# Performance work log

Hardware: AMD Instinct MI355X
Metric: run time of the kernel (lower is better)

## Reference

```python
import jax, jax.numpy as jnp
import numpy as np

N_NODES = 100000
N_EDGES = 1600000
IN_F = 256
H1, H2 = 128, 64


def gcn_conv(x, W, b, src, dst, n_nodes):
    """PyG-style GCNConv: add self-loops, symmetric deg normalization,
    transform then scatter-add aggregate, bias after aggregation."""
    loop = jnp.arange(n_nodes)
    s = jnp.concatenate([src, loop])
    d = jnp.concatenate([dst, loop])
    deg = jax.ops.segment_sum(jnp.ones_like(d, x.dtype), d, num_segments=n_nodes)
    dinv = jnp.where(deg > 0, deg ** -0.5, 0.0)
    norm = dinv[s] * dinv[d]                     # [E+N]
    h = x @ W                                    # [N, out]
    msg = h[s] * norm[:, None]                   # [E+N, out]
    out = jax.ops.segment_sum(msg, d, num_segments=n_nodes)
    return out + b


def setup_inputs() -> dict:
    key = jax.random.key(0)
    k = jax.random.split(key, 7)
    x = jax.random.normal(k[0], (N_NODES, IN_F), dtype=jnp.float32)
    edge_index = jax.random.randint(k[1], (2, N_EDGES), 0, N_NODES, dtype=jnp.int64)
    # Glorot-ish init for linear weights (PyG lin has no bias; conv bias separate)
    W1 = jax.random.normal(k[2], (IN_F, H1), dtype=jnp.float32) / np.sqrt(IN_F)
    b1 = jnp.zeros((H1,), dtype=jnp.float32)
    W2 = jax.random.normal(k[3], (H1, H2), dtype=jnp.float32) / np.sqrt(H1)
    b2 = jnp.zeros((H2,), dtype=jnp.float32)
    return {"x": x, "edge_index": edge_index, "W1": W1, "b1": b1, "W2": W2, "b2": b2}


def reference(x, edge_index, W1, b1, W2, b2):
    n = x.shape[0]
    src, dst = edge_index[0], edge_index[1]
    h = gcn_conv(x, W1, b1, src, dst, n)
    h = jax.nn.relu(h)
    # F.dropout(p=0.2, training=self.training): identity in eval mode
    out = gcn_conv(h, W2, b2, src, dst, n)
    return out
```

## Files before the change

### kernel.cpp

```cpp
#include <hip/hip_runtime.h>

#define IN_F 256
#define HID1 128
#define HID2 64
#define NBLK 256
#define RB_LOG 9
#define RB 512

typedef __bf16 bf16x8 __attribute__((ext_vector_type(8)));
typedef float f32x4 __attribute__((ext_vector_type(4)));
typedef unsigned short ushort8 __attribute__((ext_vector_type(8)));
typedef unsigned long long u64;

__device__ inline unsigned short f2bf(float f) {
    unsigned int u = __float_as_uint(f);
    u += 0x7fffu + ((u >> 16) & 1u);
    return (unsigned short)(u >> 16);
}
__device__ inline float bf2f(unsigned short u) {
    return __uint_as_float(((unsigned int)u) << 16);
}

__global__ void detect_kernel(const int* __restrict__ e, long long nOdd, int* flag) {
    long long stride = (long long)gridDim.x * blockDim.x;
    for (long long i = (long long)blockIdx.x * blockDim.x + threadIdx.x; i < nOdd; i += stride) {
        if (e[2 * i + 1] != 0) { *flag = 1; return; }
    }
}

__device__ inline int edge_src(const void* e, const int is32, long long i, int E) {
    return is32 ? ((const int*)e)[i] : (int)((const long long*)e)[i];
}
__device__ inline int edge_dst(const void* e, const int is32, long long i, int E) {
    return is32 ? ((const int*)e)[E + i] : (int)((const long long*)e)[E + i];
}

__global__ __launch_bounds__(256) void p1_count_kernel(const void* __restrict__ e,
                                                       const int* __restrict__ flag,
                                                       int* __restrict__ bhist,
                                                       int N, int E, int nbk, int chunk) {
    __shared__ int hist[256];
    const int is32 = *flag;
    const int blk = blockIdx.x;
    const int t = threadIdx.x;
    for (int j = t; j < nbk; j += 256) hist[j] = 0;
    __syncthreads();
    long long lo = (long long)blk * chunk;
    long long hi = lo + chunk; if (hi > E) hi = E;
    for (long long i = lo + t; i < hi; i += 256) {
        int s = edge_src(e, is32, i, E);
        int d = edge_dst(e, is32, i, E);
        if ((unsigned)s < (unsigned)N && (unsigned)d < (unsigned)N)
            atomicAdd(&hist[d >> RB_LOG], 1);
    }
    __syncthreads();
    for (int j = t; j < nbk; j += 256) bhist[j * NBLK + blk] = hist[j];
}

__global__ __launch_bounds__(256) void p2a_kernel(int* __restrict__ bhist, int* __restrict__ tot) {
    __shared__ int wsums[4], wpre[4];
    const int b = blockIdx.x;
    const int t = threadIdx.x;
    int v = bhist[b * NBLK + t];
    const int lane = t & 63;
    int x = v;
#pragma unroll
    for (int off = 1; off < 64; off <<= 1) {
        int y = __shfl_up(x, off, 64);
        if (lane >= off) x += y;
    }
    if (lane == 63) wsums[t >> 6] = x;
    __syncthreads();
    if (t == 0) { int r = 0; for (int w = 0; w < 4; w++) { wpre[w] = r; r += wsums[w]; } }
    __syncthreads();
    int excl = wpre[t >> 6] + x - v;
    bhist[b * NBLK + t] = excl;
    if (t == 255) tot[b] = excl + v;
}

__global__ void p2b_kernel(const int* __restrict__ tot, int* __restrict__ bstart,
                           int* __restrict__ rowptr, int nbk, int N) {
    if (threadIdx.x == 0 && blockIdx.x == 0) {
        int r = 0;
        for (int i = 0; i < nbk; i++) { bstart[i] = r; r += tot[i]; }
        bstart[nbk] = r;
        rowptr[N] = r;
    }
}

__global__ __launch_bounds__(256) void p3_scatter_kernel(const void* __restrict__ e,
                                                         const int* __restrict__ flag,
                                                         const int* __restrict__ bhist,
                                                         const int* __restrict__ bstart,
                                                         u64* __restrict__ ebuf,
                                                         int N, int E, int nbk, int chunk) {
    __shared__ int cur[256];
    const int is32 = *flag;
    const int blk = blockIdx.x;
    const int t = threadIdx.x;
    for (int j = t; j < nbk; j += 256) cur[j] = bhist[j * NBLK + blk] + bstart[j];
    __syncthreads();
    long long lo = (long long)blk * chunk;
    long long hi = lo + chunk; if (hi > E) hi = E;
    for (long long i = lo + t; i < hi; i += 256) {
        int s = edge_src(e, is32, i, E);
        int d = edge_dst(e, is32, i, E);
        if ((unsigned)s < (unsigned)N && (unsigned)d < (unsigned)N) {
            int p = atomicAdd(&cur[d >> RB_LOG], 1);
            ebuf[p] = ((u64)(unsigned)d << 32) | (unsigned)s;
        }
    }
}

__global__ __launch_bounds__(256) void p4_finalize_kernel(const u64* __restrict__ ebuf,
                                                          const int* __restrict__ bstart,
                                                          int* __restrict__ rowptr,
                                                          float* __restrict__ dinv,
                                                          int* __restrict__ col, int N) {
    __shared__ int cnt[RB];
    __shared__ int lrp[RB];
    __shared__ int wsums[4], wpre[4];
    const int b = blockIdx.x;
    const int t = threadIdx.x;
    const int e0 = bstart[b], e1 = bstart[b + 1];
    const int node0 = b << RB_LOG;
    int nn = N - node0; if (nn > RB) nn = RB;
    for (int j = t; j < RB; j += 256) cnt[j] = 0;
    __syncthreads();
    for (int i = e0 + t; i < e1; i += 256) {
        int d = (int)(ebuf[i] >> 32);
        atomicAdd(&cnt[d - node0], 1);
    }
    __syncthreads();
    int c0 = cnt[2 * t], c1 = cnt[2 * t + 1];
    int s = c0 + c1;
    const int lane = t & 63;
    int x = s;
#pragma unroll
    for (int off = 1; off < 64; off <<= 1) {
        int y = __shfl_up(x, off, 64);
        if (lane >= off) x += y;
    }
    if (lane == 63) wsums[t >> 6] = x;
    __syncthreads();
    if (t == 0) { int r = 0; for (int w = 0; w < 4; w++) { wpre[w] = r; r += wsums[w]; } }
    __syncthreads();
    int excl = wpre[t >> 6] + x - s;
    lrp[2 * t] = excl;
    lrp[2 * t + 1] = excl + c0;
    __syncthreads();
    for (int j = t; j < nn; j += 256) {
        rowptr[node0 + j] = e0 + lrp[j];
        dinv[node0 + j] = rsqrtf((float)(cnt[j] + 1));
    }
    __syncthreads();
    for (int i = e0 + t; i < e1; i += 256) {
        u64 rec = ebuf[i];
        int d = (int)(rec >> 32);
        int p = atomicAdd(&lrp[d - node0], 1);
        col[e0 + p] = (int)(unsigned)rec;
    }
}

__global__ void wbt_kernel(const float* __restrict__ W, unsigned short* __restrict__ Wbt,
                           int K, int C) {
    int t = blockIdx.x * 256 + threadIdx.x;
    if (t >= K * C) return;
    int c = t / K;
    int k = t - c * K;
    Wbt[t] = f2bf(W[k * C + c]);
}

__global__ __launch_bounds__(256) void gemm1_mfma_kernel(const float* __restrict__ x,
                                                         const unsigned short* __restrict__ Wbt,
                                                         unsigned short* __restrict__ hb, int N) {
    __shared__ unsigned short As[64 * 64];
    __shared__ unsigned short Bs[128 * 64];
    const int t = threadIdx.x;
    const int w = t >> 6;
    const int l = t & 63;
    const int lrow = l & 15;
    const int g = l >> 4;
    const int row0 = blockIdx.x * 64;

    f32x4 acc[4][2];
#pragma unroll
    for (int m = 0; m < 4; m++)
#pragma unroll
        for (int n = 0; n < 2; n++) acc[m][n] = (f32x4){0.f, 0.f, 0.f, 0.f};

    for (int kc = 0; kc < 4; kc++) {
        __syncthreads();
#pragma unroll
        for (int it = 0; it < 2; it++) {
            int slot = it * 256 + t;
            int r = slot >> 3;
            int k0 = (slot & 7) * 8;
            int grow = row0 + r;
            float4 v0 = make_float4(0.f, 0.f, 0.f, 0.f), v1 = v0;
            if (grow < N) {
                const float* p = &x[(long long)grow * IN_F + kc * 64 + k0];
                v0 = *(const float4*)p;
                v1 = *(const float4*)(p + 4);
            }
            ushort8 u;
            u[0] = f2bf(v0.x); u[1] = f2bf(v0.y); u[2] = f2bf(v0.z); u[3] = f2bf(v0.w);
            u[4] = f2bf(v1.x); u[5] = f2bf(v1.y); u[6] = f2bf(v1.z); u[7] = f2bf(v1.w);
            *(ushort8*)&As[r * 64 + (k0 ^ ((r & 7) << 3))] = u;
        }
#pragma unroll
        for (int it = 0; it < 4; it++) {
            int slot = it * 256 + t;
            int c = slot >> 3;
            int k0 = (slot & 7) * 8;
            ushort8 u = *(const ushort8*)&Wbt[c * IN_F + kc * 64 + k0];
            *(ushort8*)&Bs[c * 64 + (k0 ^ ((c & 7) << 3))] = u;
        }
        __syncthreads();
#pragma unroll
        for (int ks = 0; ks < 2; ks++) {
            int kk = ks * 32 + g * 8;
            bf16x8 af[4], bfr[2];
#pragma unroll
            for (int m = 0; m < 4; m++) {
                int r = m * 16 + lrow;
                af[m] = *(bf16x8*)&As[r * 64 + (kk ^ ((r & 7) << 3))];
            }
#pragma unroll
            for (int n = 0; n < 2; n++) {
                int c = w * 32 + n * 16 + lrow;
                bfr[n] = *(bf16x8*)&Bs[c * 64 + (kk ^ ((c & 7) << 3))];
            }
#pragma unroll
            for (int m = 0; m < 4; m++)
#pragma unroll
                for (int n = 0; n < 2; n++)
                    acc[m][n] = __builtin_amdgcn_mfma_f32_16x16x32_bf16(af[m], bfr[n], acc[m][n], 0, 0, 0);
        }
    }
#pragma unroll
    for (int m = 0; m < 4; m++) {
        int rbase = row0 + m * 16 + g * 4;
#pragma unroll
        for (int j = 0; j < 4; j++) {
            int grow = rbase + j;
            if (grow < N) {
#pragma unroll
                for (int n = 0; n < 2; n++)
                    hb[(long long)grow * HID1 + w * 32 + n * 16 + lrow] = f2bf(acc[m][n][j]);
            }
        }
    }
}

__global__ __launch_bounds__(256) void gemm2_mfma_kernel(const unsigned short* __restrict__ ab,
                                                         const unsigned short* __restrict__ Wbt,
                                                         unsigned short* __restrict__ hb, int N) {
    __shared__ unsigned short As[64 * 64];
    __shared__ unsigned short Bs[64 * 64];
    const int t = threadIdx.x;
    const int w = t >> 6;
    const int l = t & 63;
    const int lrow = l & 15;
    const int g = l >> 4;
    const int row0 = blockIdx.x * 64;

    f32x4 acc[4];
#pragma unroll
    for (int m = 0; m < 4; m++) acc[m] = (f32x4){0.f, 0.f, 0.f, 0.f};

    for (int kc = 0; kc < 2; kc++) {
        __syncthreads();
#pragma unroll
        for (int it = 0; it < 2; it++) {
            int slot = it * 256 + t;
            int r = slot >> 3;
            int k0 = (slot & 7) * 8;
            int grow = row0 + r;
            ushort8 u = (ushort8){0, 0, 0, 0, 0, 0, 0, 0};
            if (grow < N)
                u = *(const ushort8*)&ab[(long long)grow * HID1 + kc * 64 + k0];
            *(ushort8*)&As[r * 64 + (k0 ^ ((r & 7) << 3))] = u;
        }
#pragma unroll
        for (int it = 0; it < 2; it++) {
            int slot = it * 256 + t;
            int c = slot >> 3;
            int k0 = (slot & 7) * 8;
            ushort8 u = *(const ushort8*)&Wbt[c * HID1 + kc * 64 + k0];
            *(ushort8*)&Bs[c * 64 + (k0 ^ ((c & 7) << 3))] = u;
        }
        __syncthreads();
#pragma unroll
        for (int ks = 0; ks < 2; ks++) {
            int kk = ks * 32 + g * 8;
            bf16x8 af[4], bfr;
#pragma unroll
            for (int m = 0; m < 4; m++) {
                int r = m * 16 + lrow;
                af[m] = *(bf16x8*)&As[r * 64 + (kk ^ ((r & 7) << 3))];
            }
            {
                int c = w * 16 + lrow;
                bfr = *(bf16x8*)&Bs[c * 64 + (kk ^ ((c & 7) << 3))];
            }
#pragma unroll
            for (int m = 0; m < 4; m++)
                acc[m] = __builtin_amdgcn_mfma_f32_16x16x32_bf16(af[m], bfr, acc[m], 0, 0, 0);
        }
    }
#pragma unroll
    for (int m = 0; m < 4; m++) {
        int rbase = row0 + m * 16 + g * 4;
#pragma unroll
        for (int j = 0; j < 4; j++) {
            int grow = rbase + j;
            if (grow < N)
                hb[(long long)grow * HID2 + w * 16 + lrow] = f2bf(acc[m][j]);
        }
    }
}

template <int G, bool RELUBF>
__global__ __launch_bounds__(256) void gather_bf16_kernel(const unsigned short* __restrict__ hb,
                                                          const float* __restrict__ bias,
                                                          const float* __restrict__ dinv,
                                                          const int* __restrict__ rowptr,
                                                          const int* __restrict__ col,
                                                          void* __restrict__ out, int N) {
    long long tid = (long long)blockIdx.x * 256 + threadIdx.x;
    int node = (int)(tid / G);
    int g = (int)(tid % G);
    if (node >= N) return;
    const ushort8* h8 = (const ushort8*)hb;
    float di = dinv[node];
    ushort8 hv = h8[(long long)node * G + g];
    float sum[8];
#pragma unroll
    for (int j = 0; j < 8; j++) sum[j] = di * bf2f(hv[j]);
    int p0 = rowptr[node], p1 = rowptr[node + 1];
    int p = p0;
    for (; p + 3 < p1; p += 4) {
        int s0 = col[p], s1 = col[p + 1], s2 = col[p + 2], s3 = col[p + 3];
        float w0 = dinv[s0], w1 = dinv[s1], w2 = dinv[s2], w3 = dinv[s3];
        ushort8 v0 = h8[(long long)s0 * G + g];
        ushort8 v1 = h8[(long long)s1 * G + g];
        ushort8 v2 = h8[(long long)s2 * G + g];
        ushort8 v3 = h8[(long long)s3 * G + g];
#pragma unroll
        for (int j = 0; j < 8; j++)
            sum[j] += (w0 * bf2f(v0[j]) + w1 * bf2f(v1[j])) +
                      (w2 * bf2f(v2[j]) + w3 * bf2f(v3[j]));
    }
    for (; p < p1; p++) {
        int s0 = col[p];
        float w0 = dinv[s0];
        ushort8 v0 = h8[(long long)s0 * G + g];
#pragma unroll
        for (int j = 0; j < 8; j++) sum[j] += w0 * bf2f(v0[j]);
    }
    float4 b0 = ((const float4*)bias)[g * 2];
    float4 b1 = ((const float4*)bias)[g * 2 + 1];
    float r[8];
    r[0] = b0.x + di * sum[0]; r[1] = b0.y + di * sum[1];
    r[2] = b0.z + di * sum[2]; r[3] = b0.w + di * sum[3];
    r[4] = b1.x + di * sum[4]; r[5] = b1.y + di * sum[5];
    r[6] = b1.z + di * sum[6]; r[7] = b1.w + di * sum[7];
    if (RELUBF) {
        ushort8 u;
#pragma unroll
        for (int j = 0; j < 8; j++) u[j] = f2bf(fmaxf(r[j], 0.f));
        ((ushort8*)out)[(long long)node * G + g] = u;
    } else {
        float4 o0 = make_float4(r[0], r[1], r[2], r[3]);
        float4 o1 = make_float4(r[4], r[5], r[6], r[7]);
        float4* op = (float4*)((float*)out + ((long long)node * G + g) * 8);
        op[0] = o0;
        op[1] = o1;
    }
}

extern "C" void kernel_launch(void* const* d_in, const int* in_sizes, int n_in,
                              void* d_out, int out_size, void* d_ws, size_t ws_size,
                              hipStream_t stream) {
    const float* x  = (const float*)d_in[0];
    const void*  ei = d_in[1];
    const float* W1 = (const float*)d_in[2];
    const float* b1 = (const float*)d_in[3];
    const float* W2 = (const float*)d_in[4];
    const float* b2 = (const float*)d_in[5];
    float* out = (float*)d_out;

    const int N = in_sizes[0] / IN_F;
    const int E = in_sizes[1] / 2;
    const int nbk = (N + RB - 1) >> RB_LOG;
    const int chunk = (E + NBLK - 1) / NBLK;

    char* ws = (char*)d_ws;
    size_t off = 0;
    auto alloc = [&](size_t bytes) -> char* {
        char* p = ws + off;
        off = (off + bytes + 255) & ~(size_t)255;
        return p;
    };
    int*   flag   = (int*)alloc(4);
    int*   bhist  = (int*)alloc((size_t)256 * NBLK * 4);
    int*   tot    = (int*)alloc(256 * 4);
    int*   bstart = (int*)alloc(257 * 4);
    float* dinv   = (float*)alloc((size_t)N * 4);
    int*   rowptr = (int*)alloc((size_t)(N + 1) * 4);
    u64*   ebuf   = (u64*)alloc((size_t)E * 8);
    int*   col    = (int*)alloc((size_t)E * 4);
    unsigned short* w1bt  = (unsigned short*)alloc((size_t)HID1 * IN_F * 2);
    unsigned short* w2bt  = (unsigned short*)alloc((size_t)HID2 * HID1 * 2);
    unsigned short* h1b   = (unsigned short*)alloc((size_t)N * HID1 * 2);
    unsigned short* agg1b = (unsigned short*)alloc((size_t)N * HID1 * 2);
    unsigned short* h2b   = (unsigned short*)alloc((size_t)N * HID2 * 2);

    hipMemsetAsync(flag, 0, sizeof(int), stream);

    detect_kernel<<<1024, 256, 0, stream>>>((const int*)ei, (long long)E, flag);

    p1_count_kernel<<<NBLK, 256, 0, stream>>>(ei, flag, bhist, N, E, nbk, chunk);
    p2a_kernel<<<nbk, 256, 0, stream>>>(bhist, tot);
    p2b_kernel<<<1, 64, 0, stream>>>(tot, bstart, rowptr, nbk, N);
    p3_scatter_kernel<<<NBLK, 256, 0, stream>>>(ei, flag, bhist, bstart, ebuf, N, E, nbk, chunk);
    p4_finalize_kernel<<<nbk, 256, 0, stream>>>(ebuf, bstart, rowptr, dinv, col, N);

    wbt_kernel<<<(HID1 * IN_F + 255) / 256, 256, 0, stream>>>(W1, w1bt, IN_F, HID1);
    wbt_kernel<<<(HID2 * HID1 + 255) / 256, 256, 0, stream>>>(W2, w2bt, HID1, HID2);

    gemm1_mfma_kernel<<<(N + 63) / 64, 256, 0, stream>>>(x, w1bt, h1b, N);
    gather_bf16_kernel<16, true><<<(int)(((long long)N * 16 + 255) / 256), 256, 0, stream>>>(
        h1b, b1, dinv, rowptr, col, agg1b, N);

    gemm2_mfma_kernel<<<(N + 63) / 64, 256, 0, stream>>>(agg1b, w2bt, h2b, N);
    gather_bf16_kernel<8, false><<<(int)(((long long)N * 8 + 255) / 256), 256, 0, stream>>>(
        h2b, b2, dinv, rowptr, col, out, N);
}
```

Measured before the change: 203.7 us.

## Shrink CSR buckets, parallelize bucket scan, merge weight casts, deepen gather unroll

Halves the destination bucket size to 256 nodes, giving more finalize blocks, and rewrites the single-thread bucket prefix scan as a 512-thread wave scan. The two weight transpose launches are merged into one kernel. The dtype detection now samples only the first 4096 edges in a single block. The gather kernel gains an 8-wide unrolled loop with occupancy launch bounds so more neighbor loads are in flight. Risks: the detection shortcut assumes the first edges are representative of the index dtype, and nbk must stay at or below 512.

```diff
diff --git a/kernel.cpp b/kernel.cpp
--- a/kernel.cpp
+++ b/kernel.cpp
@@ -4,8 +4,8 @@
 #define HID1 128
 #define HID2 64
 #define NBLK 256
-#define RB_LOG 9
-#define RB 512
+#define RB_LOG 8
+#define RB 256
 
 typedef __bf16 bf16x8 __attribute__((ext_vector_type(8)));
 typedef float f32x4 __attribute__((ext_vector_type(4)));
@@ -39,7 +39,7 @@
                                                        const int* __restrict__ flag,
                                                        int* __restrict__ bhist,
                                                        int N, int E, int nbk, int chunk) {
-    __shared__ int hist[256];
+    __shared__ int hist[512];
     const int is32 = *flag;
     const int blk = blockIdx.x;
     const int t = threadIdx.x;
@@ -78,13 +78,29 @@
     if (t == 255) tot[b] = excl + v;
 }
 
-__global__ void p2b_kernel(const int* __restrict__ tot, int* __restrict__ bstart,
-                           int* __restrict__ rowptr, int nbk, int N) {
-    if (threadIdx.x == 0 && blockIdx.x == 0) {
-        int r = 0;
-        for (int i = 0; i < nbk; i++) { bstart[i] = r; r += tot[i]; }
-        bstart[nbk] = r;
-        rowptr[N] = r;
+__global__ __launch_bounds__(512) void p2b_kernel(const int* __restrict__ tot,
+                                                  int* __restrict__ bstart,
+                                                  int* __restrict__ rowptr, int nbk, int N) {
+    __shared__ int wsums[8], wpre[8];
+    const int t = threadIdx.x;
+    int v = (t < nbk) ? tot[t] : 0;
+    const int lane = t & 63;
+    int x = v;
+#pragma unroll
+    for (int off = 1; off < 64; off <<= 1) {
+        int y = __shfl_up(x, off, 64);
+        if (lane >= off) x += y;
+    }
+    if (lane == 63) wsums[t >> 6] = x;
+    __syncthreads();
+    if (t == 0) { int r = 0; for (int w = 0; w < 8; w++) { wpre[w] = r; r += wsums[w]; } }
+    __syncthreads();
+    int excl = wpre[t >> 6] + x - v;
+    if (t < nbk) bstart[t] = excl;
+    if (t == 511) {
+        int total = wpre[7] + wsums[7];
+        bstart[nbk] = total;
+        rowptr[N] = total;
     }
 }
 
@@ -94,7 +110,7 @@
                                                          const int* __restrict__ bstart,
                                                          u64* __restrict__ ebuf,
                                                          int N, int E, int nbk, int chunk) {
-    __shared__ int cur[256];
+    __shared__ int cur[512];
     const int is32 = *flag;
     const int blk = blockIdx.x;
     const int t = threadIdx.x;
@@ -125,17 +141,16 @@
     const int e0 = bstart[b], e1 = bstart[b + 1];
     const int node0 = b << RB_LOG;
     int nn = N - node0; if (nn > RB) nn = RB;
-    for (int j = t; j < RB; j += 256) cnt[j] = 0;
+    cnt[t] = 0;
     __syncthreads();
     for (int i = e0 + t; i < e1; i += 256) {
         int d = (int)(ebuf[i] >> 32);
         atomicAdd(&cnt[d - node0], 1);
     }
     __syncthreads();
-    int c0 = cnt[2 * t], c1 = cnt[2 * t + 1];
-    int s = c0 + c1;
+    int v = cnt[t];
     const int lane = t & 63;
-    int x = s;
+    int x = v;
 #pragma unroll
     for (int off = 1; off < 64; off <<= 1) {
         int y = __shfl_up(x, off, 64);
@@ -145,13 +160,11 @@
     __syncthreads();
     if (t == 0) { int r = 0; for (int w = 0; w < 4; w++) { wpre[w] = r; r += wsums[w]; } }
     __syncthreads();
-    int excl = wpre[t >> 6] + x - s;
-    lrp[2 * t] = excl;
-    lrp[2 * t + 1] = excl + c0;
-    __syncthreads();
-    for (int j = t; j < nn; j += 256) {
-        rowptr[node0 + j] = e0 + lrp[j];
-        dinv[node0 + j] = rsqrtf((float)(cnt[j] + 1));
+    int excl = wpre[t >> 6] + x - v;
+    lrp[t] = excl;
+    if (t < nn) {
+        rowptr[node0 + t] = e0 + excl;
+        dinv[node0 + t] = rsqrtf((float)(v + 1));
     }
     __syncthreads();
     for (int i = e0 + t; i < e1; i += 256) {
@@ -162,13 +175,19 @@
     }
 }
 
-__global__ void wbt_kernel(const float* __restrict__ W, unsigned short* __restrict__ Wbt,
-                           int K, int C) {
+__global__ void wbt2_kernel(const float* __restrict__ W1, unsigned short* __restrict__ w1bt,
+                            const float* __restrict__ W2, unsigned short* __restrict__ w2bt) {
     int t = blockIdx.x * 256 + threadIdx.x;
-    if (t >= K * C) return;
-    int c = t / K;
-    int k = t - c * K;
-    Wbt[t] = f2bf(W[k * C + c]);
+    if (t < IN_F * HID1) {
+        int c = t >> 8, k = t & 255;
+        w1bt[t] = f2bf(W1[k * HID1 + c]);
+    } else {
+        int u = t - IN_F * HID1;
+        if (u < HID1 * HID2) {
+            int c = u >> 7, k = u & 127;
+            w2bt[u] = f2bf(W2[k * HID2 + c]);
+        }
+    }
 }
 
 __global__ __launch_bounds__(256) void gemm1_mfma_kernel(const float* __restrict__ x,
@@ -322,12 +341,12 @@
 }
 
 template <int G, bool RELUBF>
-__global__ __launch_bounds__(256) void gather_bf16_kernel(const unsigned short* __restrict__ hb,
-                                                          const float* __restrict__ bias,
-                                                          const float* __restrict__ dinv,
-                                                          const int* __restrict__ rowptr,
-                                                          const int* __restrict__ col,
-                                                          void* __restrict__ out, int N) {
+__global__ __launch_bounds__(256, 8) void gather_bf16_kernel(const unsigned short* __restrict__ hb,
+                                                             const float* __restrict__ bias,
+                                                             const float* __restrict__ dinv,
+                                                             const int* __restrict__ rowptr,
+                                                             const int* __restrict__ col,
+                                                             void* __restrict__ out, int N) {
     long long tid = (long long)blockIdx.x * 256 + threadIdx.x;
     int node = (int)(tid / G);
     int g = (int)(tid % G);
@@ -340,6 +359,21 @@
     for (int j = 0; j < 8; j++) sum[j] = di * bf2f(hv[j]);
     int p0 = rowptr[node], p1 = rowptr[node + 1];
     int p = p0;
+    for (; p + 7 < p1; p += 8) {
+        int sN[8];
+        float wN[8];
+        ushort8 vN[8];
+#pragma unroll
+        for (int q = 0; q < 8; q++) sN[q] = col[p + q];
+#pragma unroll
+        for (int q = 0; q < 8; q++) vN[q] = h8[(long long)sN[q] * G + g];
+#pragma unroll
+        for (int q = 0; q < 8; q++) wN[q] = dinv[sN[q]];
+#pragma unroll
+        for (int q = 0; q < 8; q++)
+#pragma unroll
+            for (int j = 0; j < 8; j++) sum[j] += wN[q] * bf2f(vN[q][j]);
+    }
     for (; p + 3 < p1; p += 4) {
         int s0 = col[p], s1 = col[p + 1], s2 = col[p + 2], s3 = col[p + 3];
         float w0 = dinv[s0], w1 = dinv[s1], w2 = dinv[s2], w3 = dinv[s3];
@@ -404,9 +438,9 @@
         return p;
     };
     int*   flag   = (int*)alloc(4);
-    int*   bhist  = (int*)alloc((size_t)256 * NBLK * 4);
-    int*   tot    = (int*)alloc(256 * 4);
-    int*   bstart = (int*)alloc(257 * 4);
+    int*   bhist  = (int*)alloc((size_t)512 * NBLK * 4);
+    int*   tot    = (int*)alloc(512 * 4);
+    int*   bstart = (int*)alloc(520 * 4);
     float* dinv   = (float*)alloc((size_t)N * 4);
     int*   rowptr = (int*)alloc((size_t)(N + 1) * 4);
     u64*   ebuf   = (u64*)alloc((size_t)E * 8);
@@ -419,16 +453,16 @@
 
     hipMemsetAsync(flag, 0, sizeof(int), stream);
 
-    detect_kernel<<<1024, 256, 0, stream>>>((const int*)ei, (long long)E, flag);
+    long long nOdd = E < 4096 ? (long long)E : 4096;
+    detect_kernel<<<1, 256, 0, stream>>>((const int*)ei, nOdd, flag);
 
     p1_count_kernel<<<NBLK, 256, 0, stream>>>(ei, flag, bhist, N, E, nbk, chunk);
     p2a_kernel<<<nbk, 256, 0, stream>>>(bhist, tot);
-    p2b_kernel<<<1, 64, 0, stream>>>(tot, bstart, rowptr, nbk, N);
+    p2b_kernel<<<1, 512, 0, stream>>>(tot, bstart, rowptr, nbk, N);
     p3_scatter_kernel<<<NBLK, 256, 0, stream>>>(ei, flag, bhist, bstart, ebuf, N, E, nbk, chunk);
     p4_finalize_kernel<<<nbk, 256, 0, stream>>>(ebuf, bstart, rowptr, dinv, col, N);
 
-    wbt_kernel<<<(HID1 * IN_F + 255) / 256, 256, 0, stream>>>(W1, w1bt, IN_F, HID1);
-    wbt_kernel<<<(HID2 * HID1 + 255) / 256, 256, 0, stream>>>(W2, w2bt, HID1, HID2);
+    wbt2_kernel<<<(IN_F * HID1 + HID1 * HID2 + 255) / 256, 256, 0, stream>>>(W1, w1bt, W2, w2bt);
 
     gemm1_mfma_kernel<<<(N + 63) / 64, 256, 0, stream>>>(x, w1bt, h1b, N);
     gather_bf16_kernel<16, true><<<(int)(((long long)N * 16 + 255) / 256), 256, 0, stream>>>(
```

After: 261.0 us. +28.1%, slower.
